# Optimization experiments

Measured on AMD Instinct MI355X. Metric: run time of the kernel, lower is better.

The kernel has to match this reference:

```python
import jax, jax.numpy as jnp
import numpy as np

D_MODEL = 1024
NUM_HEADS = 16
HEAD_DIM = D_MODEL // NUM_HEADS


def setup_inputs() -> dict:
    key = jax.random.key(0)
    ks = jax.random.split(key, 10)
    B, S, D = 2, 2048, D_MODEL
    s = 1.0 / np.sqrt(D)
    return {
        "x": jax.random.normal(ks[0], (B, S, D), dtype=jnp.float32),
        "q_w": jax.random.normal(ks[1], (D, D), dtype=jnp.float32) * s,
        "q_b": jnp.zeros((D,), dtype=jnp.float32),
        "k_w": jax.random.normal(ks[2], (D, D), dtype=jnp.float32) * s,
        "k_b": jnp.zeros((D,), dtype=jnp.float32),
        "v_w": jax.random.normal(ks[3], (D, D), dtype=jnp.float32) * s,
        "v_b": jnp.zeros((D,), dtype=jnp.float32),
        "out_w": jax.random.normal(ks[4], (D, D), dtype=jnp.float32) * s,
        "out_b": jnp.zeros((D,), dtype=jnp.float32),
        "evidence_scale": jnp.ones((1,), dtype=jnp.float32),
        "evidence_bias": jnp.zeros((1,), dtype=jnp.float32),
    }


def reference(x, q_w, q_b, k_w, k_b, v_w, v_b, out_w, out_b, evidence_scale, evidence_bias):
    B, S, D = x.shape
    H, Hd = NUM_HEADS, HEAD_DIM

    def proj(w, b):  # torch Linear: x @ w.T + b, then split heads -> [B,H,S,Hd]
        y = jnp.einsum('bsd,ed->bse', x, w) + b
        return y.reshape(B, S, H, Hd).transpose(0, 2, 1, 3)

    Q = proj(q_w, q_b)
    K = proj(k_w, k_b)
    V = proj(v_w, v_b)

    scores = jnp.einsum('bhqd,bhkd->bhqk', Q, K) / np.sqrt(Hd)  # [B,H,S,S]
    evidence = jnp.exp(scores) * evidence_scale + 1.0 + evidence_bias
    denom = evidence.sum(axis=-1, keepdims=True)                # [B,H,S,1]
    uncertainty = S / denom                                     # [B,H,S,1]
    probs = evidence / denom

    attn = jnp.einsum('bhqk,bhkd->bhqd', probs, V)              # [B,H,S,Hd]
    attn = attn.transpose(0, 2, 1, 3).reshape(B, S, D)
    output = jnp.einsum('bsd,ed->bse', attn, out_w) + out_b
    return output, jnp.squeeze(uncertainty, -1)
```

## Files before the change

kernel.cpp:

```cpp
#include <hip/hip_runtime.h>

typedef __attribute__((ext_vector_type(8))) short bf16x8;
typedef __attribute__((ext_vector_type(4))) float f32x4;
typedef unsigned short ushort_t;

constexpr int Dm  = 1024;
constexpr int NH  = 16;
constexpr int HD  = 64;
constexpr int SQ  = 2048;
constexpr int BB  = 2;
constexpr int MM  = BB * SQ;

__device__ __forceinline__ ushort_t f2bf(float f) {
    unsigned int u = __float_as_uint(f);
    u += 0x7FFFu + ((u >> 16) & 1u);
    return (ushort_t)(u >> 16);
}

__device__ __forceinline__ void gld16(const void* g, void* l) {
    __builtin_amdgcn_global_load_lds(
        (const __attribute__((address_space(1))) void*)g,
        (__attribute__((address_space(3))) void*)l, 16, 0, 0);
}

__global__ void cast_all(const float4* __restrict__ x,  const float4* __restrict__ qw,
                         const float4* __restrict__ kw, const float4* __restrict__ vw,
                         const float4* __restrict__ ow,
                         uint2* __restrict__ xb,  uint2* __restrict__ qwb,
                         uint2* __restrict__ kwb, uint2* __restrict__ vwb,
                         uint2* __restrict__ owb)
{
    int i = blockIdx.x * 256 + threadIdx.x;
    const float4* src; uint2* dst; int off;
    if      (i < 1048576) { src = x;  dst = xb;  off = i; }
    else if (i < 1310720) { src = qw; dst = qwb; off = i - 1048576; }
    else if (i < 1572864) { src = kw; dst = kwb; off = i - 1310720; }
    else if (i < 1835008) { src = vw; dst = vwb; off = i - 1572864; }
    else                  { src = ow; dst = owb; off = i - 1835008; }
    float4 v = src[off];
    uint2 o;
    o.x = (unsigned)f2bf(v.x) | ((unsigned)f2bf(v.y) << 16);
    o.y = (unsigned)f2bf(v.z) | ((unsigned)f2bf(v.w) << 16);
    dst[off] = o;
}

template<int TM, typename EPI>
__device__ __forceinline__ void gemm_core(const ushort_t* __restrict__ A,
                                          const ushort_t* __restrict__ W,
                                          const float* __restrict__ bias,
                                          int n0, int m0, EPI epi)
{
    constexpr int AF = TM / 32;
    __shared__ ushort_t As[2][TM * 32];
    __shared__ ushort_t Ws[2][128 * 32];
    const int t    = threadIdx.x;
    const int lane = t & 63, w = t >> 6;
    const int lm   = lane & 15, quad = lane >> 4;
    const int wm   = w & 1, wn = w >> 1;

    const f32x4 fz = {0.f, 0.f, 0.f, 0.f};
    f32x4 acc[AF][4];
#pragma unroll
    for (int mi = 0; mi < AF; ++mi)
#pragma unroll
        for (int ni = 0; ni < 4; ++ni) acc[mi][ni] = fz;

    float bsv[4];
#pragma unroll
    for (int ni = 0; ni < 4; ++ni) bsv[ni] = bias[n0 + wn * 64 + ni * 16 + lm];

    auto stage = [&](int k0, int b) {
#pragma unroll
        for (int j = 0; j < TM / 64; ++j) {
            int s = t + 256 * j;
            gld16(A + (size_t)(m0 + (s >> 2)) * 1024 + k0 + (s & 3) * 8, &As[b][s * 8]);
        }
#pragma unroll
        for (int j = 0; j < 2; ++j) {
            int s = t + 256 * j;
            gld16(W + (size_t)(n0 + (s >> 2)) * 1024 + k0 + (s & 3) * 8, &Ws[b][s * 8]);
        }
    };

    stage(0, 0);
    int cur = 0;
    for (int k0 = 0; k0 < 1024; k0 += 32) {
        __syncthreads();
        if (k0 + 32 < 1024) stage(k0 + 32, cur ^ 1);

        bf16x8 af[AF], bfr[4];
#pragma unroll
        for (int mi = 0; mi < AF; ++mi)
            af[mi] = *(const bf16x8*)&As[cur][(wm * (TM / 2) + mi * 16 + lm) * 32 + quad * 8];
#pragma unroll
        for (int ni = 0; ni < 4; ++ni)
            bfr[ni] = *(const bf16x8*)&Ws[cur][(wn * 64 + ni * 16 + lm) * 32 + quad * 8];
#pragma unroll
        for (int mi = 0; mi < AF; ++mi)
#pragma unroll
            for (int ni = 0; ni < 4; ++ni)
                acc[mi][ni] = __builtin_amdgcn_mfma_f32_16x16x32_bf16(
                                  af[mi], bfr[ni], acc[mi][ni], 0, 0, 0);
        cur ^= 1;
    }

#pragma unroll
    for (int mi = 0; mi < AF; ++mi)
#pragma unroll
        for (int ni = 0; ni < 4; ++ni)
#pragma unroll
            for (int r = 0; r < 4; ++r) {
                const int m = m0 + wm * (TM / 2) + mi * 16 + quad * 4 + r;
                const int n = n0 + wn * 64 + ni * 16 + lm;
                epi(m, n, acc[mi][ni][r] + bsv[ni]);
            }
}

__global__ __launch_bounds__(256) void gemm_qkv(
    const ushort_t* __restrict__ xb,
    const ushort_t* __restrict__ qwb, const float* __restrict__ qb,
    const ushort_t* __restrict__ kwb, const float* __restrict__ kb,
    const ushort_t* __restrict__ vwb, const float* __restrict__ vb,
    ushort_t* __restrict__ Qb, ushort_t* __restrict__ Kb, ushort_t* __restrict__ Vb)
{
    const int z = blockIdx.z;
    const ushort_t* W   = (z == 0) ? qwb : (z == 1) ? kwb : vwb;
    const float*    bias = (z == 0) ? qb  : (z == 1) ? kb  : vb;
    ushort_t*       dst  = (z == 0) ? Qb  : (z == 1) ? Kb  : Vb;
    const int n0 = blockIdx.x * 128, m0 = blockIdx.y * 128;
    const bool vt = (z == 2);

    gemm_core<128>(xb, W, bias, n0, m0, [&](int m, int n, float v) {
        const int b = m >> 11, s = m & 2047, h = n >> 6, hd = n & 63;
        const size_t idx = vt ? ((size_t)((b * NH + h) * 64 + hd) * SQ + s)
                              : ((size_t)((b * NH + h) * SQ + s) * 64 + hd);
        dst[idx] = f2bf(v);
    });
}

__global__ __launch_bounds__(256) void gemm_out(
    const ushort_t* __restrict__ Ab, const ushort_t* __restrict__ owb,
    const float* __restrict__ ob, float* __restrict__ out)
{
    const int n0 = blockIdx.x * 128, m0 = blockIdx.y * 64;
    gemm_core<64>(Ab, owb, ob, n0, m0, [&](int m, int n, float v) {
        out[(size_t)m * 1024 + n] = v;
    });
}

__global__ __launch_bounds__(256) void attn_mfma(const ushort_t* __restrict__ Qg,
                                                 const ushort_t* __restrict__ Kg,
                                                 const ushort_t* __restrict__ Vtg,
                                                 const float* __restrict__ esc,
                                                 const float* __restrict__ ebi,
                                                 ushort_t* __restrict__ Ab,
                                                 float* __restrict__ unc)
{
    __shared__ __align__(16) ushort_t Kbuf[2][4096];
    __shared__ __align__(16) ushort_t Vbuf[2][4096];
    __shared__ __align__(16) ushort_t Es[4][16 * 40];

    const int t    = threadIdx.x;
    const int lane = t & 63, w = t >> 6;
    const int lm   = lane & 15, quad = lane >> 4;
    const int qt   = blockIdx.x & 31;
    const int bh   = blockIdx.x >> 5;
    const int q0   = qt * 64;

    const float scale = esc[0];
    const float bias1 = 1.0f + ebi[0];

    bf16x8 qa[2];
#pragma unroll
    for (int kc = 0; kc < 2; ++kc)
        qa[kc] = *(const bf16x8*)(Qg + (size_t)(bh * SQ + q0 + w * 16 + lm) * 64
                                  + kc * 32 + quad * 8);

    const f32x4 fz = {0.f, 0.f, 0.f, 0.f};
    f32x4 acc[4];
#pragma unroll
    for (int nd = 0; nd < 4; ++nd) acc[nd] = fz;
    float drow[4] = {0.f, 0.f, 0.f, 0.f};

    auto stage = [&](int kt, int b) {
        const ushort_t* kg = Kg + (size_t)(bh * SQ + kt * 64 + w * 16 + lm) * 64 + quad * 8;
        gld16(kg,      &Kbuf[b][(w * 2 + 0) * 512]);
        gld16(kg + 32, &Kbuf[b][(w * 2 + 1) * 512]);
        const ushort_t* vg = Vtg + (size_t)bh * 64 * SQ + (size_t)(w * 16 + lm) * SQ
                           + kt * 64 + quad * 8;
        gld16(vg,      &Vbuf[b][(w * 2 + 0) * 512]);
        gld16(vg + 32, &Vbuf[b][(w * 2 + 1) * 512]);
    };

    stage(0, 0);
    int cur = 0;
    for (int kt = 0; kt < 32; ++kt) {
        __syncthreads();
        if (kt + 1 < 32) stage(kt + 1, cur ^ 1);
        const ushort_t* Kc = Kbuf[cur];
        const ushort_t* Vc = Vbuf[cur];
        ushort_t* EsW = &Es[w][0];

#pragma unroll
        for (int hc = 0; hc < 2; ++hc) {
#pragma unroll
            for (int ni = 0; ni < 2; ++ni) {
                f32x4 s = fz;
#pragma unroll
                for (int kc = 0; kc < 2; ++kc) {
                    bf16x8 kb = *(const bf16x8*)&Kc[((hc * 2 + ni) * 2 + kc) * 512 + lane * 8];
                    s = __builtin_amdgcn_mfma_f32_16x16x32_bf16(qa[kc], kb, s, 0, 0, 0);
                }
#pragma unroll
                for (int r = 0; r < 4; ++r) {
                    float ev = __expf(s[r] * 0.125f) * scale + bias1;
                    drow[r] += ev;
                    EsW[(quad * 4 + r) * 40 + ni * 16 + lm] = f2bf(ev);
                }
            }
            bf16x8 ea = *(const bf16x8*)&EsW[lm * 40 + quad * 8];
#pragma unroll
            for (int nd = 0; nd < 4; ++nd) {
                bf16x8 vb = *(const bf16x8*)&Vc[(nd * 2 + hc) * 512 + lane * 8];
                acc[nd] = __builtin_amdgcn_mfma_f32_16x16x32_bf16(ea, vb, acc[nd], 0, 0, 0);
            }
        }
        cur ^= 1;
    }

#pragma unroll
    for (int r = 0; r < 4; ++r) {
        float d = drow[r];
        d += __shfl_xor(d, 1, 64);
        d += __shfl_xor(d, 2, 64);
        d += __shfl_xor(d, 4, 64);
        d += __shfl_xor(d, 8, 64);
        drow[r] = d;
    }
    if (lm == 0) {
#pragma unroll
        for (int r = 0; r < 4; ++r)
            unc[(size_t)bh * SQ + q0 + w * 16 + quad * 4 + r] = (float)SQ / drow[r];
    }

    const int b = bh >> 4, h = bh & 15;
    float di[4];
#pragma unroll
    for (int r = 0; r < 4; ++r) di[r] = 1.0f / drow[r];
#pragma unroll
    for (int nd = 0; nd < 4; ++nd)
#pragma unroll
        for (int r = 0; r < 4; ++r) {
            const int q = w * 16 + quad * 4 + r;
            Ab[(size_t)(b * SQ + q0 + q) * Dm + h * 64 + nd * 16 + lm]
                = f2bf(acc[nd][r] * di[r]);
        }
}

extern "C" void kernel_launch(void* const* d_in, const int* in_sizes, int n_in,
                              void* d_out, int out_size, void* d_ws, size_t ws_size,
                              hipStream_t stream)
{
    const float* x   = (const float*)d_in[0];
    const float* qw  = (const float*)d_in[1];
    const float* qb  = (const float*)d_in[2];
    const float* kw  = (const float*)d_in[3];
    const float* kb  = (const float*)d_in[4];
    const float* vw  = (const float*)d_in[5];
    const float* vb  = (const float*)d_in[6];
    const float* ow  = (const float*)d_in[7];
    const float* ob  = (const float*)d_in[8];
    const float* esc = (const float*)d_in[9];
    const float* ebi = (const float*)d_in[10];

    float* out = (float*)d_out;
    float* unc = out + (size_t)MM * Dm;

    ushort_t* xb  = (ushort_t*)d_ws;
    ushort_t* qwb = (ushort_t*)((char*)d_ws + (8u  << 20));
    ushort_t* kwb = (ushort_t*)((char*)d_ws + (10u << 20));
    ushort_t* vwb = (ushort_t*)((char*)d_ws + (12u << 20));
    ushort_t* owb = (ushort_t*)((char*)d_ws + (14u << 20));
    ushort_t* Vb  = (ushort_t*)((char*)d_ws + (16u << 20));
    ushort_t* Ab  = xb;

    ushort_t* Qb = (ushort_t*)d_out;
    ushort_t* Kb = Qb + (size_t)MM * Dm;

    cast_all<<<dim3(2097152 / 256), dim3(256), 0, stream>>>(
        (const float4*)x, (const float4*)qw, (const float4*)kw,
        (const float4*)vw, (const float4*)ow,
        (uint2*)xb, (uint2*)qwb, (uint2*)kwb, (uint2*)vwb, (uint2*)owb);

    gemm_qkv<<<dim3(Dm / 128, MM / 128, 3), dim3(256), 0, stream>>>(
        xb, qwb, qb, kwb, kb, vwb, vb, Qb, Kb, Vb);

    attn_mfma<<<dim3(BB * NH * (SQ / 64)), dim3(256), 0, stream>>>(
        Qb, Kb, Vb, esc, ebi, Ab, unc);

    gemm_out<<<dim3(Dm / 128, MM / 64), dim3(256), 0, stream>>>(Ab, owb, ob, out);
}
```

Baseline: 225.4 us.

## Keep attention evidence in registers via transposed MFMA and lane swizzle, drop LDS staging

```diff
diff --git a/kernel.cpp b/kernel.cpp
--- a/kernel.cpp
+++ b/kernel.cpp
@@ -2,6 +2,7 @@
 
 typedef __attribute__((ext_vector_type(8))) short bf16x8;
 typedef __attribute__((ext_vector_type(4))) float f32x4;
+typedef __attribute__((ext_vector_type(4))) unsigned int u32x4;
 typedef unsigned short ushort_t;
 
 constexpr int Dm  = 1024;
@@ -129,8 +130,10 @@
     ushort_t*       dst  = (z == 0) ? Qb  : (z == 1) ? Kb  : Vb;
     const int n0 = blockIdx.x * 128, m0 = blockIdx.y * 128;
     const bool vt = (z == 2);
+    const float qs = (z == 0) ? 0.125f : 1.0f;
 
     gemm_core<128>(xb, W, bias, n0, m0, [&](int m, int n, float v) {
+        v *= qs;
         const int b = m >> 11, s = m & 2047, h = n >> 6, hd = n & 63;
         const size_t idx = vt ? ((size_t)((b * NH + h) * 64 + hd) * SQ + s)
                               : ((size_t)((b * NH + h) * SQ + s) * 64 + hd);
@@ -158,7 +161,6 @@
 {
     __shared__ __align__(16) ushort_t Kbuf[2][4096];
     __shared__ __align__(16) ushort_t Vbuf[2][4096];
-    __shared__ __align__(16) ushort_t Es[4][16 * 40];
 
     const int t    = threadIdx.x;
     const int lane = t & 63, w = t >> 6;
@@ -176,85 +178,95 @@
         qa[kc] = *(const bf16x8*)(Qg + (size_t)(bh * SQ + q0 + w * 16 + lm) * 64
                                   + kc * 32 + quad * 8);
 
+    bf16x8 onesA;
+#pragma unroll
+    for (int j = 0; j < 8; ++j) onesA[j] = (short)0x3F80;
+
     const f32x4 fz = {0.f, 0.f, 0.f, 0.f};
     f32x4 acc[4];
 #pragma unroll
     for (int nd = 0; nd < 4; ++nd) acc[nd] = fz;
-    float drow[4] = {0.f, 0.f, 0.f, 0.f};
+    f32x4 acc1 = fz;
+
+    const int vq = ((quad & 1) << 4) + ((quad >> 1) << 3);
 
     auto stage = [&](int kt, int b) {
         const ushort_t* kg = Kg + (size_t)(bh * SQ + kt * 64 + w * 16 + lm) * 64 + quad * 8;
         gld16(kg,      &Kbuf[b][(w * 2 + 0) * 512]);
         gld16(kg + 32, &Kbuf[b][(w * 2 + 1) * 512]);
         const ushort_t* vg = Vtg + (size_t)bh * 64 * SQ + (size_t)(w * 16 + lm) * SQ
-                           + kt * 64 + quad * 8;
+                           + kt * 64 + vq;
         gld16(vg,      &Vbuf[b][(w * 2 + 0) * 512]);
         gld16(vg + 32, &Vbuf[b][(w * 2 + 1) * 512]);
     };
 
     stage(0, 0);
     int cur = 0;
+    const bool odd = (quad & 1) != 0;
     for (int kt = 0; kt < 32; ++kt) {
         __syncthreads();
         if (kt + 1 < 32) stage(kt + 1, cur ^ 1);
         const ushort_t* Kc = Kbuf[cur];
         const ushort_t* Vc = Vbuf[cur];
-        ushort_t* EsW = &Es[w][0];
 
 #pragma unroll
         for (int hc = 0; hc < 2; ++hc) {
-#pragma unroll
-            for (int ni = 0; ni < 2; ++ni) {
-                f32x4 s = fz;
-#pragma unroll
-                for (int kc = 0; kc < 2; ++kc) {
-                    bf16x8 kb = *(const bf16x8*)&Kc[((hc * 2 + ni) * 2 + kc) * 512 + lane * 8];
-                    s = __builtin_amdgcn_mfma_f32_16x16x32_bf16(qa[kc], kb, s, 0, 0, 0);
-                }
-#pragma unroll
-                for (int r = 0; r < 4; ++r) {
-                    float ev = __expf(s[r] * 0.125f) * scale + bias1;
-                    drow[r] += ev;
-                    EsW[(quad * 4 + r) * 40 + ni * 16 + lm] = f2bf(ev);
-                }
+            f32x4 st0 = fz, st1 = fz;
+#pragma unroll
+            for (int kc = 0; kc < 2; ++kc) {
+                bf16x8 kb0 = *(const bf16x8*)&Kc[((hc * 2 + 0) * 2 + kc) * 512 + lane * 8];
+                bf16x8 kb1 = *(const bf16x8*)&Kc[((hc * 2 + 1) * 2 + kc) * 512 + lane * 8];
+                st0 = __builtin_amdgcn_mfma_f32_16x16x32_bf16(kb0, qa[kc], st0, 0, 0, 0);
+                st1 = __builtin_amdgcn_mfma_f32_16x16x32_bf16(kb1, qa[kc], st1, 0, 0, 0);
             }
-            bf16x8 ea = *(const bf16x8*)&EsW[lm * 40 + quad * 8];
+            unsigned pk0[2], pk1[2];
+#pragma unroll
+            for (int p = 0; p < 2; ++p) {
+                float a0 = fmaf(__expf(st0[2 * p]),     scale, bias1);
+                float a1 = fmaf(__expf(st0[2 * p + 1]), scale, bias1);
+                float b0 = fmaf(__expf(st1[2 * p]),     scale, bias1);
+                float b1 = fmaf(__expf(st1[2 * p + 1]), scale, bias1);
+                asm("v_cvt_pk_bf16_f32 %0, %1, %2" : "=v"(pk0[p]) : "v"(a0), "v"(a1));
+                asm("v_cvt_pk_bf16_f32 %0, %1, %2" : "=v"(pk1[p]) : "v"(b0), "v"(b1));
+            }
+            unsigned keep0 = odd ? pk1[0] : pk0[0];
+            unsigned keep1 = odd ? pk1[1] : pk0[1];
+            unsigned send0 = odd ? pk0[0] : pk1[0];
+            unsigned send1 = odd ? pk0[1] : pk1[1];
+            unsigned recv0 = (unsigned)__builtin_amdgcn_ds_swizzle((int)send0, 0x401F);
+            unsigned recv1 = (unsigned)__builtin_amdgcn_ds_swizzle((int)send1, 0x401F);
+            u32x4 fv;
+            fv[0] = odd ? recv0 : keep0;
+            fv[1] = odd ? recv1 : keep1;
+            fv[2] = odd ? keep0 : recv0;
+            fv[3] = odd ? keep1 : recv1;
+            bf16x8 eb = __builtin_bit_cast(bf16x8, fv);
 #pragma unroll
             for (int nd = 0; nd < 4; ++nd) {
-                bf16x8 vb = *(const bf16x8*)&Vc[(nd * 2 + hc) * 512 + lane * 8];
-                acc[nd] = __builtin_amdgcn_mfma_f32_16x16x32_bf16(ea, vb, acc[nd], 0, 0, 0);
+                bf16x8 va = *(const bf16x8*)&Vc[(nd * 2 + hc) * 512 + lane * 8];
+                acc[nd] = __builtin_amdgcn_mfma_f32_16x16x32_bf16(va, eb, acc[nd], 0, 0, 0);
             }
+            acc1 = __builtin_amdgcn_mfma_f32_16x16x32_bf16(onesA, eb, acc1, 0, 0, 0);
         }
         cur ^= 1;
     }
 
-#pragma unroll
-    for (int r = 0; r < 4; ++r) {
-        float d = drow[r];
-        d += __shfl_xor(d, 1, 64);
-        d += __shfl_xor(d, 2, 64);
-        d += __shfl_xor(d, 4, 64);
-        d += __shfl_xor(d, 8, 64);
-        drow[r] = d;
+    const float di = 1.0f / acc1[0];
+    if (quad == 0)
+        unc[(size_t)bh * SQ + q0 + w * 16 + lm] = (float)SQ * di;
+
+    const int b = bh >> 4, h = bh & 15;
+    const size_t arow = (size_t)(b * SQ + q0 + w * 16 + lm) * Dm + h * 64;
+#pragma unroll
+    for (int nd = 0; nd < 4; ++nd) {
+        float o0 = acc[nd][0] * di, o1 = acc[nd][1] * di;
+        float o2 = acc[nd][2] * di, o3 = acc[nd][3] * di;
+        unsigned lo, hi;
+        asm("v_cvt_pk_bf16_f32 %0, %1, %2" : "=v"(lo) : "v"(o0), "v"(o1));
+        asm("v_cvt_pk_bf16_f32 %0, %1, %2" : "=v"(hi) : "v"(o2), "v"(o3));
+        uint2 ov; ov.x = lo; ov.y = hi;
+        *(uint2*)&Ab[arow + nd * 16 + quad * 4] = ov;
     }
-    if (lm == 0) {
-#pragma unroll
-        for (int r = 0; r < 4; ++r)
-            unc[(size_t)bh * SQ + q0 + w * 16 + quad * 4 + r] = (float)SQ / drow[r];
-    }
-
-    const int b = bh >> 4, h = bh & 15;
-    float di[4];
-#pragma unroll
-    for (int r = 0; r < 4; ++r) di[r] = 1.0f / drow[r];
-#pragma unroll
-    for (int nd = 0; nd < 4; ++nd)
-#pragma unroll
-        for (int r = 0; r < 4; ++r) {
-            const int q = w * 16 + quad * 4 + r;
-            Ab[(size_t)(b * SQ + q0 + q) * Dm + h * 64 + nd * 16 + lm]
-                = f2bf(acc[nd][r] * di[r]);
-        }
 }
 
 extern "C" void kernel_launch(void* const* d_in, const int* in_sizes, int n_in,
```

Measured after the change: 220.5 us. 2.1% less time.

## Restructure attention to split keys across waves and keep probabilities in registers

Applied to the files above, without the earlier changes.

```diff
diff --git a/kernel.cpp b/kernel.cpp
--- a/kernel.cpp
+++ b/kernel.cpp
@@ -1,7 +1,10 @@
 #include <hip/hip_runtime.h>
 
 typedef __attribute__((ext_vector_type(8))) short bf16x8;
+typedef __attribute__((ext_vector_type(4))) short bf16x4;
 typedef __attribute__((ext_vector_type(4))) float f32x4;
+typedef __attribute__((ext_vector_type(4))) unsigned int u32x4;
+typedef __attribute__((ext_vector_type(2))) unsigned int u32x2;
 typedef unsigned short ushort_t;
 
 constexpr int Dm  = 1024;
@@ -129,8 +132,10 @@
     ushort_t*       dst  = (z == 0) ? Qb  : (z == 1) ? Kb  : Vb;
     const int n0 = blockIdx.x * 128, m0 = blockIdx.y * 128;
     const bool vt = (z == 2);
+    const float qs = (z == 0) ? 0.125f : 1.0f;
 
     gemm_core<128>(xb, W, bias, n0, m0, [&](int m, int n, float v) {
+        v *= qs;
         const int b = m >> 11, s = m & 2047, h = n >> 6, hd = n & 63;
         const size_t idx = vt ? ((size_t)((b * NH + h) * 64 + hd) * SQ + s)
                               : ((size_t)((b * NH + h) * SQ + s) * 64 + hd);
@@ -148,17 +153,17 @@
     });
 }
 
-__global__ __launch_bounds__(256) void attn_mfma(const ushort_t* __restrict__ Qg,
-                                                 const ushort_t* __restrict__ Kg,
-                                                 const ushort_t* __restrict__ Vtg,
-                                                 const float* __restrict__ esc,
-                                                 const float* __restrict__ ebi,
-                                                 ushort_t* __restrict__ Ab,
-                                                 float* __restrict__ unc)
-{
-    __shared__ __align__(16) ushort_t Kbuf[2][4096];
-    __shared__ __align__(16) ushort_t Vbuf[2][4096];
-    __shared__ __align__(16) ushort_t Es[4][16 * 40];
+__global__ __launch_bounds__(256, 3) void attn_mfma(const ushort_t* __restrict__ Qg,
+                                                    const ushort_t* __restrict__ Kg,
+                                                    const ushort_t* __restrict__ Vtg,
+                                                    const float* __restrict__ esc,
+                                                    const float* __restrict__ ebi,
+                                                    ushort_t* __restrict__ Ab,
+                                                    float* __restrict__ unc)
+{
+    __shared__ __align__(16) ushort_t smem[20480];
+    ushort_t* Kb0 = smem;
+    ushort_t* Vb0 = smem + 8192;
 
     const int t    = threadIdx.x;
     const int lane = t & 63, w = t >> 6;
@@ -170,91 +175,171 @@
     const float scale = esc[0];
     const float bias1 = 1.0f + ebi[0];
 
-    bf16x8 qa[2];
-#pragma unroll
-    for (int kc = 0; kc < 2; ++kc)
-        qa[kc] = *(const bf16x8*)(Qg + (size_t)(bh * SQ + q0 + w * 16 + lm) * 64
-                                  + kc * 32 + quad * 8);
+    bf16x8 qa[4][2];
+#pragma unroll
+    for (int i = 0; i < 4; ++i)
+#pragma unroll
+        for (int kc = 0; kc < 2; ++kc)
+            qa[i][kc] = *(const bf16x8*)(Qg + (size_t)(bh * SQ + q0 + ((w ^ i) * 16) + lm) * 64
+                                         + kc * 32 + quad * 8);
 
     const f32x4 fz = {0.f, 0.f, 0.f, 0.f};
-    f32x4 acc[4];
-#pragma unroll
-    for (int nd = 0; nd < 4; ++nd) acc[nd] = fz;
+    f32x4 acc[4][4];
+#pragma unroll
+    for (int i = 0; i < 4; ++i)
+#pragma unroll
+        for (int nd = 0; nd < 4; ++nd) acc[i][nd] = fz;
     float drow[4] = {0.f, 0.f, 0.f, 0.f};
 
     auto stage = [&](int kt, int b) {
         const ushort_t* kg = Kg + (size_t)(bh * SQ + kt * 64 + w * 16 + lm) * 64 + quad * 8;
-        gld16(kg,      &Kbuf[b][(w * 2 + 0) * 512]);
-        gld16(kg + 32, &Kbuf[b][(w * 2 + 1) * 512]);
-        const ushort_t* vg = Vtg + (size_t)bh * 64 * SQ + (size_t)(w * 16 + lm) * SQ
-                           + kt * 64 + quad * 8;
-        gld16(vg,      &Vbuf[b][(w * 2 + 0) * 512]);
-        gld16(vg + 32, &Vbuf[b][(w * 2 + 1) * 512]);
+        gld16(kg,      Kb0 + b * 4096 + (w * 2 + 0) * 512);
+        gld16(kg + 32, Kb0 + b * 4096 + (w * 2 + 1) * 512);
+#pragma unroll
+        for (int j = 0; j < 2; ++j) {
+            const int s  = j * 256 + t;
+            const int d  = s >> 3;
+            const int kc = (s ^ (s >> 3)) & 7;
+            gld16(Vtg + (size_t)bh * 64 * SQ + (size_t)d * SQ + kt * 64 + kc * 8,
+                  Vb0 + b * 4096 + (j * 256 + w * 64) * 8);
+        }
     };
+
+    const int vbase = (lm * 128 + w * 32 + quad * 8) ^ ((lm & 7) << 4);
 
     stage(0, 0);
     int cur = 0;
-    for (int kt = 0; kt < 32; ++kt) {
+    unsigned pkA[4][2], pkB[4][2];
+    bf16x4 vaA[4], vaB[4];
+
+    for (int ktp = 0; ktp < 16; ++ktp) {
         __syncthreads();
-        if (kt + 1 < 32) stage(kt + 1, cur ^ 1);
-        const ushort_t* Kc = Kbuf[cur];
-        const ushort_t* Vc = Vbuf[cur];
-        ushort_t* EsW = &Es[w][0];
-
-#pragma unroll
-        for (int hc = 0; hc < 2; ++hc) {
-#pragma unroll
-            for (int ni = 0; ni < 2; ++ni) {
-                f32x4 s = fz;
-#pragma unroll
-                for (int kc = 0; kc < 2; ++kc) {
-                    bf16x8 kb = *(const bf16x8*)&Kc[((hc * 2 + ni) * 2 + kc) * 512 + lane * 8];
-                    s = __builtin_amdgcn_mfma_f32_16x16x32_bf16(qa[kc], kb, s, 0, 0, 0);
-                }
-#pragma unroll
-                for (int r = 0; r < 4; ++r) {
-                    float ev = __expf(s[r] * 0.125f) * scale + bias1;
-                    drow[r] += ev;
-                    EsW[(quad * 4 + r) * 40 + ni * 16 + lm] = f2bf(ev);
+        stage(2 * ktp + 1, cur ^ 1);
+        {
+            const ushort_t* Kc = Kb0 + cur * 4096;
+            const char*     Vcb = (const char*)(Vb0 + cur * 4096);
+            bf16x8 kf0 = *(const bf16x8*)&Kc[(w * 2 + 0) * 512 + lane * 8];
+            bf16x8 kf1 = *(const bf16x8*)&Kc[(w * 2 + 1) * 512 + lane * 8];
+#pragma unroll
+            for (int nd = 0; nd < 4; ++nd)
+                vaA[nd] = *(const bf16x4*)(Vcb + vbase + nd * 2048);
+#pragma unroll
+            for (int i = 0; i < 4; ++i) {
+                f32x4 st = fz;
+                st = __builtin_amdgcn_mfma_f32_16x16x32_bf16(kf0, qa[i][0], st, 0, 0, 0);
+                st = __builtin_amdgcn_mfma_f32_16x16x32_bf16(kf1, qa[i][1], st, 0, 0, 0);
+                float e0 = fmaf(__expf(st[0]), scale, bias1);
+                float e1 = fmaf(__expf(st[1]), scale, bias1);
+                float e2 = fmaf(__expf(st[2]), scale, bias1);
+                float e3 = fmaf(__expf(st[3]), scale, bias1);
+                drow[i] += (e0 + e1) + (e2 + e3);
+                asm("v_cvt_pk_bf16_f32 %0, %1, %2" : "=v"(pkA[i][0]) : "v"(e0), "v"(e1));
+                asm("v_cvt_pk_bf16_f32 %0, %1, %2" : "=v"(pkA[i][1]) : "v"(e2), "v"(e3));
+            }
+        }
+        cur ^= 1;
+
+        __syncthreads();
+        if (2 * ktp + 2 < 32) stage(2 * ktp + 2, cur ^ 1);
+        {
+            const ushort_t* Kc = Kb0 + cur * 4096;
+            const char*     Vcb = (const char*)(Vb0 + cur * 4096);
+            bf16x8 kf0 = *(const bf16x8*)&Kc[(w * 2 + 0) * 512 + lane * 8];
+            bf16x8 kf1 = *(const bf16x8*)&Kc[(w * 2 + 1) * 512 + lane * 8];
+#pragma unroll
+            for (int nd = 0; nd < 4; ++nd)
+                vaB[nd] = *(const bf16x4*)(Vcb + vbase + nd * 2048);
+#pragma unroll
+            for (int i = 0; i < 4; ++i) {
+                f32x4 st = fz;
+                st = __builtin_amdgcn_mfma_f32_16x16x32_bf16(kf0, qa[i][0], st, 0, 0, 0);
+                st = __builtin_amdgcn_mfma_f32_16x16x32_bf16(kf1, qa[i][1], st, 0, 0, 0);
+                float e0 = fmaf(__expf(st[0]), scale, bias1);
+                float e1 = fmaf(__expf(st[1]), scale, bias1);
+                float e2 = fmaf(__expf(st[2]), scale, bias1);
+                float e3 = fmaf(__expf(st[3]), scale, bias1);
+                drow[i] += (e0 + e1) + (e2 + e3);
+                asm("v_cvt_pk_bf16_f32 %0, %1, %2" : "=v"(pkB[i][0]) : "v"(e0), "v"(e1));
+                asm("v_cvt_pk_bf16_f32 %0, %1, %2" : "=v"(pkB[i][1]) : "v"(e2), "v"(e3));
+            }
+#pragma unroll
+            for (int nd = 0; nd < 4; ++nd) {
+                u32x2 a2 = __builtin_bit_cast(u32x2, vaA[nd]);
+                u32x2 b2 = __builtin_bit_cast(u32x2, vaB[nd]);
+                u32x4 uv; uv[0] = a2[0]; uv[1] = a2[1]; uv[2] = b2[0]; uv[3] = b2[1];
+                bf16x8 va8 = __builtin_bit_cast(bf16x8, uv);
+#pragma unroll
+                for (int i = 0; i < 4; ++i) {
+                    u32x4 ue; ue[0] = pkA[i][0]; ue[1] = pkA[i][1];
+                    ue[2] = pkB[i][0]; ue[3] = pkB[i][1];
+                    bf16x8 eb = __builtin_bit_cast(bf16x8, ue);
+                    acc[i][nd] = __builtin_amdgcn_mfma_f32_16x16x32_bf16(va8, eb, acc[i][nd], 0, 0, 0);
                 }
             }
-            bf16x8 ea = *(const bf16x8*)&EsW[lm * 40 + quad * 8];
-#pragma unroll
-            for (int nd = 0; nd < 4; ++nd) {
-                bf16x8 vb = *(const bf16x8*)&Vc[(nd * 2 + hc) * 512 + lane * 8];
-                acc[nd] = __builtin_amdgcn_mfma_f32_16x16x32_bf16(ea, vb, acc[nd], 0, 0, 0);
-            }
         }
         cur ^= 1;
     }
 
-#pragma unroll
-    for (int r = 0; r < 4; ++r) {
-        float d = drow[r];
-        d += __shfl_xor(d, 1, 64);
-        d += __shfl_xor(d, 2, 64);
-        d += __shfl_xor(d, 4, 64);
-        d += __shfl_xor(d, 8, 64);
-        drow[r] = d;
-    }
-    if (lm == 0) {
-#pragma unroll
-        for (int r = 0; r < 4; ++r)
-            unc[(size_t)bh * SQ + q0 + w * 16 + quad * 4 + r] = (float)SQ / drow[r];
-    }
+    float* S = (float*)smem;
+    __syncthreads();
+    {
+        float* R = S + w * 2560 + lane * 20;
+#pragma unroll
+        for (int nd = 0; nd < 4; ++nd) {
+            *(f32x4*)(R + nd * 4)        = acc[1][nd];
+            *(f32x4*)(R + 1280 + nd * 4) = acc[3][nd];
+        }
+        R[16]        = drow[1];
+        R[1280 + 16] = drow[3];
+    }
+    __syncthreads();
+    {
+        const float* P = S + (w ^ 1) * 2560 + lane * 20;
+#pragma unroll
+        for (int nd = 0; nd < 4; ++nd) {
+            acc[0][nd] += *(const f32x4*)(P + nd * 4);
+            acc[2][nd] += *(const f32x4*)(P + 1280 + nd * 4);
+        }
+        drow[0] += P[16];
+        drow[2] += P[1280 + 16];
+    }
+    __syncthreads();
+    {
+        float* R = S + w * 1280 + lane * 20;
+#pragma unroll
+        for (int nd = 0; nd < 4; ++nd)
+            *(f32x4*)(R + nd * 4) = acc[2][nd];
+        R[16] = drow[2];
+    }
+    __syncthreads();
+    {
+        const float* P = S + (w ^ 2) * 1280 + lane * 20;
+#pragma unroll
+        for (int nd = 0; nd < 4; ++nd)
+            acc[0][nd] += *(const f32x4*)(P + nd * 4);
+        drow[0] += P[16];
+    }
+
+    float d = drow[0];
+    d += __shfl_xor(d, 16, 64);
+    d += __shfl_xor(d, 32, 64);
+    const float di = 1.0f / d;
+
+    if (quad == 0)
+        unc[(size_t)bh * SQ + q0 + w * 16 + lm] = (float)SQ * di;
 
     const int b = bh >> 4, h = bh & 15;
-    float di[4];
-#pragma unroll
-    for (int r = 0; r < 4; ++r) di[r] = 1.0f / drow[r];
-#pragma unroll
-    for (int nd = 0; nd < 4; ++nd)
-#pragma unroll
-        for (int r = 0; r < 4; ++r) {
-            const int q = w * 16 + quad * 4 + r;
-            Ab[(size_t)(b * SQ + q0 + q) * Dm + h * 64 + nd * 16 + lm]
-                = f2bf(acc[nd][r] * di[r]);
-        }
+    const size_t arow = (size_t)(b * SQ + q0 + w * 16 + lm) * Dm + h * 64;
+#pragma unroll
+    for (int nd = 0; nd < 4; ++nd) {
+        float o0 = acc[0][nd][0] * di, o1 = acc[0][nd][1] * di;
+        float o2 = acc[0][nd][2] * di, o3 = acc[0][nd][3] * di;
+        unsigned lo, hi;
+        asm("v_cvt_pk_bf16_f32 %0, %1, %2" : "=v"(lo) : "v"(o0), "v"(o1));
+        asm("v_cvt_pk_bf16_f32 %0, %1, %2" : "=v"(hi) : "v"(o2), "v"(o3));
+        uint2 ov; ov.x = lo; ov.y = hi;
+        *(uint2*)&Ab[arow + nd * 16 + quad * 4] = ov;
+    }
 }
 
 extern "C" void kernel_launch(void* const* d_in, const int* in_sizes, int n_in,
```

Result: slower. 256.9 us (+14.0%).
